# Kernel tuning notes

Hardware: AMD Instinct MI355X
Metric: run time of the kernel (lower is better)

## Reference

```python
import jax, jax.numpy as jnp
import numpy as np

N_NODES = 50000
N_EDGES = 800000
HIDDEN = 128
HEADS = 8
HEAD_DIM = HIDDEN // HEADS
N_LAYERS = 2
BATCH = 64
INPUT = 300


def setup_inputs() -> dict:
    key = jax.random.key(0)
    ks = jax.random.split(key, 10)
    s = 0.05
    word_embed_matrix = jax.random.normal(ks[0], (N_NODES, INPUT), dtype=jnp.float32)
    edge_index = jax.random.randint(ks[1], (2, N_EDGES), 0, N_NODES, dtype=jnp.int32)
    target_idx = jax.random.randint(ks[2], (BATCH,), 0, N_NODES, dtype=jnp.int32)
    # labels: first half positive, second half negative (batch/2 pos as in original loss)
    label_id = jnp.concatenate([jnp.ones(BATCH // 2, jnp.int32), jnp.zeros(BATCH // 2, jnp.int32)])
    lin1_W = jax.random.normal(ks[3], (INPUT, HIDDEN), dtype=jnp.float32) * s
    lin1_b = jnp.zeros((HIDDEN,), jnp.float32)
    gat_W = jax.random.normal(ks[4], (N_LAYERS, HIDDEN, HIDDEN), dtype=jnp.float32) * s
    gat_att_src = jax.random.normal(ks[5], (N_LAYERS, HEADS, HEAD_DIM), dtype=jnp.float32) * s
    gat_att_dst = jax.random.normal(ks[6], (N_LAYERS, HEADS, HEAD_DIM), dtype=jnp.float32) * s
    gat_bias = jnp.zeros((N_LAYERS, HIDDEN), jnp.float32)
    lin3_W = jax.random.normal(ks[7], (HIDDEN, 1), dtype=jnp.float32) * s
    lin3_b = jnp.zeros((1,), jnp.float32)
    return {"word_embed_matrix": word_embed_matrix, "edge_index": edge_index,
            "target_idx": target_idx, "label_id": label_id,
            "lin1_W": lin1_W, "lin1_b": lin1_b, "gat_W": gat_W,
            "gat_att_src": gat_att_src, "gat_att_dst": gat_att_dst,
            "gat_bias": gat_bias, "lin3_W": lin3_W, "lin3_b": lin3_b}


def gat_layer(x, src, dst, W, a_src, a_dst, b):
    # x: [N, HIDDEN]; src/dst: [E'] (self loops included)
    N = x.shape[0]
    h = (x @ W).reshape(N, HEADS, HEAD_DIM)               # [N,H,C]
    alpha_src = jnp.sum(h * a_src, axis=-1)               # [N,H]
    alpha_dst = jnp.sum(h * a_dst, axis=-1)               # [N,H]
    e = jax.nn.leaky_relu(alpha_src[src] + alpha_dst[dst], 0.2)  # [E',H]
    # softmax over incoming edges of each dst node (segment softmax)
    emax = jax.ops.segment_max(e, dst, num_segments=N)    # [N,H]
    ee = jnp.exp(e - emax[dst])
    denom = jax.ops.segment_sum(ee, dst, num_segments=N)  # [N,H]
    alpha = ee / denom[dst]                               # [E',H]
    msg = h[src] * alpha[:, :, None]                      # [E',H,C]
    out = jax.ops.segment_sum(msg, dst, num_segments=N)   # [N,H,C]
    return out.reshape(N, HIDDEN) + b


def reference(word_embed_matrix, edge_index, target_idx, label_id,
              lin1_W, lin1_b, gat_W, gat_att_src, gat_att_dst, gat_bias,
              lin3_W, lin3_b):
    N = word_embed_matrix.shape[0]
    # add self loops (PyG GATConv default)
    loop = jnp.arange(N, dtype=edge_index.dtype)
    src = jnp.concatenate([edge_index[0], loop])
    dst = jnp.concatenate([edge_index[1], loop])
    x = word_embed_matrix @ lin1_W + lin1_b
    for i in range(N_LAYERS):
        x = jax.nn.elu(gat_layer(x, src, dst, gat_W[i], gat_att_src[i], gat_att_dst[i], gat_bias[i]))
    target_embed = x[target_idx]                          # [B, HIDDEN]
    total_score = (target_embed @ lin3_W + lin3_b)[:, 0]  # [B]
    # labels are [1]*B/2 + [0]*B/2 (static layout, matches label_id)
    half = BATCH // 2
    pos_score = total_score[:half]
    neg_score = total_score[half:]
    loss = jnp.mean(jax.nn.relu(1.0 - (pos_score - neg_score)))
    return (total_score, loss)
```

## Files before the change

### kernel.cpp

```cpp
#include <hip/hip_runtime.h>
#include <math.h>

#define N_NODES 50000
#define N_EDGESI 800000
#define E_TOT   850000
#define HIDDEN  128
#define HEADS   8
#define HEAD_DIM 16
#define INPUT   300
#define BATCH   64

#define NR    128
#define RSZ   391
#define CAP   8192
#define CHUNK 2048
#define NSB   ((E_TOT + CHUNK - 1)/CHUNK)
#define FCAP  8192

typedef __bf16 bf16_t;
typedef bf16_t bf16x8 __attribute__((ext_vector_type(8)));
typedef bf16_t bf16x2 __attribute__((ext_vector_type(2)));
typedef float  f32x4  __attribute__((ext_vector_type(4)));
typedef float  f32x2  __attribute__((ext_vector_type(2)));

__global__ void wa_kernel(const float* __restrict__ W, const float* __restrict__ as,
                          const float* __restrict__ ad, float* __restrict__ Wa){
    int k = threadIdx.x;
    #pragma unroll
    for (int j = 0; j < 8; j++){
        float s1 = 0.f, s2 = 0.f;
        #pragma unroll
        for (int d = 0; d < 16; d++){
            float wv = W[k*128 + j*16 + d];
            s1 += wv * as[j*16 + d];
            s2 += wv * ad[j*16 + d];
        }
        Wa[k*16 + j]     = s1;
        Wa[k*16 + 8 + j] = s2;
    }
}

template<int K_REAL, int K_PAD, int NCOL>
__global__ void fused_pack_kernel(const float* __restrict__ W1, const float* __restrict__ Wg,
                                  const float* __restrict__ Wa, const float* __restrict__ b1,
                                  bf16_t* __restrict__ bF, float* __restrict__ bcomb){
    int idx = blockIdx.x*256 + threadIdx.x;
    if (idx < NCOL){
        float s = 0.f;
        for (int d = 0; d < 128; d++)
            s += b1[d] * ((idx < 128) ? Wg[d*128 + idx] : Wa[d*16 + (idx - 128)]);
        bcomb[idx] = s;
    }
    if (idx >= K_PAD*NCOL) return;
    int k = idx / NCOL, col = idx % NCOL;
    float v = 0.f;
    if (k < K_REAL){
        const float* w1r = W1 + k*128;
        if (col < 128){
            for (int m = 0; m < 128; m++) v += w1r[m] * Wg[m*128 + col];
        } else {
            int jj = col - 128;
            for (int m = 0; m < 128; m++) v += w1r[m] * Wa[m*16 + jj];
        }
    }
    int o = ((k >> 3)*NCOL + col)*8 + (k & 7);
    bF[o] = (bf16_t)v;
}

template<int K_REAL, int K_PAD, int NCOL, bool ALPHA>
__global__ void pack_b_kernel(const float* __restrict__ B128, const float* __restrict__ as,
                              const float* __restrict__ ad, bf16_t* __restrict__ bHi){
    int idx = blockIdx.x*256 + threadIdx.x;
    if (idx >= K_PAD*NCOL) return;
    int k = idx / NCOL, col = idx % NCOL;
    float v = 0.f;
    if (k < K_REAL){
        if (!ALPHA || col < 128){
            v = B128[k*128 + col];
        } else {
            int jj = col - 128;
            const float* a = (jj < 8) ? (as + jj*16) : (ad + (jj-8)*16);
            const float* wrow = B128 + k*128 + (jj & 7)*16;
            float s = 0.f;
            #pragma unroll
            for (int d = 0; d < 16; d++) s += wrow[d]*a[d];
            v = s;
        }
    }
    int o = ((k >> 3)*NCOL + col)*8 + (k & 7);
    bHi[o] = (bf16_t)v;
}

template<int K_REAL, int K_PAD, int NT, int GH, int PD, bool A_BF16, bool BIAS_EPI, bool ALPHA, bool OUT8, bool INDIRECT>
__global__ __launch_bounds__(256)
void mfma_gemm6_kernel(const void* __restrict__ A_, const bf16_t* __restrict__ bHi,
                       const float* __restrict__ bias, void* __restrict__ outP,
                       float* __restrict__ asrc_out, float* __restrict__ adst_out, int M,
                       const int* __restrict__ rlist, const int* __restrict__ cnt_ptr)
{
    constexpr int NCOL   = NT * 16;
    constexpr int KSTEPS = K_PAD / 32;
    constexpr int KSPP   = GH / 4;
    constexpr int NPASS  = KSTEPS / KSPP;
    constexpr int PELEM  = GH * NCOL * 8;
    constexpr int SIT    = PELEM / 2048;
    static_assert(KSPP * NPASS == KSTEPS && SIT * 2048 == PELEM, "");
    __shared__ bf16_t blds[PELEM];

    int mEff = M;
    if (INDIRECT) mEff = cnt_ptr[0];
    if ((int)(blockIdx.x*64) >= mEff) return;

    int tid = threadIdx.x, lane = tid & 63, w = tid >> 6;
    int l15 = lane & 15, lg = lane >> 4;
    int m0 = (blockIdx.x*4 + w) * 16;
    int mrow = m0 + l15; if (mrow >= mEff) mrow = mEff - 1;
    int arow_idx = INDIRECT ? rlist[mrow] : mrow;

    const float*  arowF = (const float*) A_ + (size_t)arow_idx*K_REAL;
    const bf16_t* arowB = (const bf16_t*)A_ + (size_t)arow_idx*K_REAL;

    float4 pva[PD], pvb[PD];
    bf16x8 pab[PD];
    #pragma unroll
    for (int i = 0; i < PD; i++){
        int k0 = i*32 + lg*8;
        if (A_BF16){
            pab[i] = *(const bf16x8*)&arowB[k0];
        } else {
            pva[i] = (k0 + 3 < K_REAL) ? *(const float4*)&arowF[k0]     : (float4){0.f,0.f,0.f,0.f};
            pvb[i] = (k0 + 7 < K_REAL) ? *(const float4*)&arowF[k0 + 4] : (float4){0.f,0.f,0.f,0.f};
        }
    }

    f32x4 acc[NT];
    #pragma unroll
    for (int c = 0; c < NT; c++) acc[c] = (f32x4){0.f,0.f,0.f,0.f};

    #pragma unroll
    for (int p = 0; p < NPASS; p++){
        const bf16_t* gB = bHi + (size_t)p*PELEM;
        if (p) __syncthreads();
        #pragma unroll
        for (int it = 0; it < SIT; it++){
            int idx = (tid + it*256)*8;
            *(bf16x8*)&blds[idx] = *(const bf16x8*)&gB[idx];
        }
        __syncthreads();

        #pragma unroll
        for (int i = 0; i < KSPP; i++){
            const int ks = p*KSPP + i;
            const int sl = ks % PD;
            bf16x8 ah;
            if (A_BF16){
                ah = pab[sl];
            } else {
                float4 va = pva[sl], vb = pvb[sl];
                float f[8] = {va.x, va.y, va.z, va.w, vb.x, vb.y, vb.z, vb.w};
                #pragma unroll
                for (int q = 0; q < 8; q++) ah[q] = (bf16_t)f[q];
            }
            if (ks + PD < KSTEPS){
                int k0 = (ks + PD)*32 + lg*8;
                if (A_BF16){
                    pab[sl] = *(const bf16x8*)&arowB[k0];
                } else {
                    pva[sl] = (k0 + 3 < K_REAL) ? *(const float4*)&arowF[k0]     : (float4){0.f,0.f,0.f,0.f};
                    pvb[sl] = (k0 + 7 < K_REAL) ? *(const float4*)&arowF[k0 + 4] : (float4){0.f,0.f,0.f,0.f};
                }
            }
            int gloc = i*4 + lg;
            const bf16_t* b_base = &blds[(gloc*NCOL + l15)*8];
            #pragma unroll
            for (int c = 0; c < NT; c++){
                bf16x8 bh = *(const bf16x8*)&b_base[c*128];
                acc[c] = __builtin_amdgcn_mfma_f32_16x16x32_bf16(ah, bh, acc[c], 0,0,0);
            }
        }
    }

    #pragma unroll
    for (int c = 0; c < 8; c++){
        int col = c*16 + l15;
        float bv = BIAS_EPI ? bias[col] : 0.f;
        #pragma unroll
        for (int r = 0; r < 4; r++){
            int m = m0 + lg*4 + r;
            if (m < mEff){
                int row = INDIRECT ? rlist[m] : m;
                float v = acc[c][r] + bv;
                if (OUT8){
                    int pk = __builtin_amdgcn_cvt_pk_fp8_f32(v, v, 0, false);
                    ((unsigned char*)outP)[(size_t)row*128 + col] = (unsigned char)(pk & 0xff);
                } else {
                    ((bf16_t*)outP)[(size_t)row*128 + col] = (bf16_t)v;
                }
            }
        }
    }
    if (ALPHA){
        float bv8 = BIAS_EPI ? bias[128 + l15] : 0.f;
        #pragma unroll
        for (int r = 0; r < 4; r++){
            int m = m0 + lg*4 + r;
            if (m < mEff){
                int row = INDIRECT ? rlist[m] : m;
                float v = acc[8][r] + bv8;
                if (l15 < 8) asrc_out[row*8 + l15]       = v;
                else         adst_out[row*8 + (l15 - 8)] = v;
            }
        }
    }
}

__global__ void zero_cnt_kernel(int* __restrict__ bucket_cnt){
    bucket_cnt[threadIdx.x] = 0;
}

__global__ __launch_bounds__(256)
void block_sort_kernel(const int* __restrict__ ei, int* __restrict__ bucket_cnt,
                       int2* __restrict__ pairs2){
    __shared__ int2 stageL[CHUNK];
    __shared__ int2 sortedL[CHUNK];
    __shared__ unsigned short binL[CHUNK];
    __shared__ int histL[NR], lstartL[NR], lcurL[NR], gofsL[NR];
    int tid = threadIdx.x, b = blockIdx.x;
    int e0 = b*CHUNK, e1 = e0 + CHUNK; if (e1 > E_TOT) e1 = E_TOT;
    int n = e1 - e0;
    if (tid < NR) histL[tid] = 0;
    __syncthreads();
    for (int i = tid; i < n; i += 256){
        int e = e0 + i;
        int s, d;
        if (e < N_EDGESI){ s = ei[e]; d = ei[N_EDGESI + e]; }
        else { s = e - N_EDGESI; d = s; }
        stageL[i] = make_int2(s, d);
        atomicAdd(&histL[d/RSZ], 1);
    }
    __syncthreads();
    if (tid < NR) lstartL[tid] = histL[tid];
    __syncthreads();
    for (int off = 1; off < NR; off <<= 1){
        int t = 0;
        if (tid < NR && tid >= off) t = lstartL[tid - off];
        __syncthreads();
        if (tid < NR) lstartL[tid] += t;
        __syncthreads();
    }
    if (tid < NR){
        int excl = lstartL[tid] - histL[tid];
        lstartL[tid] = excl;
        lcurL[tid]   = excl;
    }
    __syncthreads();
    for (int i = tid; i < n; i += 256){
        int2 pr = stageL[i];
        int bb = pr.y / RSZ;
        int pos = atomicAdd(&lcurL[bb], 1);
        sortedL[pos] = pr;
        binL[pos] = (unsigned short)bb;
    }
    __syncthreads();
    if (tid < NR) gofsL[tid] = atomicAdd(&bucket_cnt[tid], histL[tid]);
    __syncthreads();
    for (int i = tid; i < n; i += 256){
        int bb = binL[i];
        int dst = bb*CAP + gofsL[bb] + (i - lstartL[bb]);
        pairs2[dst] = sortedL[i];
    }
}

__global__ void rbase_scan_kernel(const int* __restrict__ bucket_cnt, int* __restrict__ rbase){
    __shared__ int s[NR];
    int t = threadIdx.x;
    s[t] = bucket_cnt[t];
    __syncthreads();
    for (int off = 1; off < NR; off <<= 1){
        int u = (t >= off) ? s[t - off] : 0;
        __syncthreads();
        s[t] += u;
        __syncthreads();
    }
    rbase[t + 1] = s[t];
    if (t == 0) rbase[0] = 0;
}

__global__ __launch_bounds__(512)
void csr_finalize_kernel(const int2* __restrict__ pairs2, const int* __restrict__ bucket_cnt,
                         const int* __restrict__ rbase, int* __restrict__ col_src,
                         int* __restrict__ row_ptr){
    __shared__ int2 pairsL[CAP];
    __shared__ int  colL[CAP];
    __shared__ int  degL[512];
    __shared__ int  startL[512];
    __shared__ int  curL[512];
    int tid = threadIdx.x, r = blockIdx.x;
    int cnt = bucket_cnt[r], base = rbase[r];
    degL[tid] = 0;
    __syncthreads();
    for (int i = tid; i < cnt; i += 512){
        int2 pr = pairs2[r*CAP + i];
        pairsL[i] = pr;
        atomicAdd(&degL[pr.y - r*RSZ], 1);
    }
    __syncthreads();
    int v = degL[tid];
    for (int off = 1; off < 512; off <<= 1){
        int u = (tid >= off) ? degL[tid - off] : 0;
        __syncthreads();
        degL[tid] += u;
        __syncthreads();
    }
    int excl = degL[tid] - v;
    startL[tid] = excl;
    curL[tid]   = excl;
    __syncthreads();
    for (int i = tid; i < cnt; i += 512){
        int2 pr = pairsL[i];
        int pos = atomicAdd(&curL[pr.y - r*RSZ], 1);
        colL[pos] = pr.x;
    }
    __syncthreads();
    for (int i = tid; i < cnt; i += 512)
        col_src[base + i] = colL[i];
    if (tid < RSZ){
        int node = r*RSZ + tid;
        if (node < N_NODES) row_ptr[node] = base + startL[tid];
    }
    if (r == NR-1 && tid == 0) row_ptr[N_NODES] = E_TOT;
}

__global__ void build_frontier_kernel(const int* __restrict__ tgt, const int* __restrict__ row_ptr,
                                      const int* __restrict__ col_src, int* __restrict__ list,
                                      int* __restrict__ fcnt){
    __shared__ int st[64], en[64], ofs[65];
    int t = threadIdx.x;
    if (t < 64){ int d = tgt[t]; st[t] = row_ptr[d]; en[t] = row_ptr[d + 1]; }
    __syncthreads();
    if (t == 0){
        int acc = 64;
        for (int i = 0; i < 64; i++){
            ofs[i] = acc;
            int n = en[i] - st[i];
            acc += n;
        }
        if (acc > FCAP) acc = FCAP;
        ofs[64] = acc;
        fcnt[0] = acc;
    }
    __syncthreads();
    if (t < 64) list[t] = tgt[t];
    for (int i = 0; i < 64; i++){
        int n = en[i] - st[i];
        int o = ofs[i];
        for (int j = t; j < n && o + j < FCAP; j += 256)
            list[o + j] = col_src[st[i] + j];
    }
}

__global__ __launch_bounds__(256)
void gat_aggregate_kernel(const int* __restrict__ row_ptr, const int* __restrict__ col_src,
                          const unsigned char* __restrict__ H8, const float* __restrict__ a_s,
                          const float* __restrict__ a_d, const float* __restrict__ bias,
                          bf16_t* __restrict__ xout, const int* __restrict__ nlist, int nn,
                          const int* __restrict__ nn_ptr){
    __shared__ float alds[4][8][65];
    int wave = threadIdx.x >> 6;
    int lane = threadIdx.x & 63;
    if (nn_ptr) nn = nn_ptr[0];
    int gid = blockIdx.x*4 + wave;
    if (gid >= nn) return;
    int d = nlist ? nlist[gid] : gid;
    int start = row_ptr[d], end = row_ptr[d + 1];
    int deg = end - start;
    int hme = lane >> 3, seg = lane & 7;

    float ad_[8];
    {
        float4 t0 = *(const float4*)&a_d[d*8];
        float4 t1 = *(const float4*)&a_d[d*8 + 4];
        ad_[0]=t0.x; ad_[1]=t0.y; ad_[2]=t0.z; ad_[3]=t0.w;
        ad_[4]=t1.x; ad_[5]=t1.y; ad_[6]=t1.z; ad_[7]=t1.w;
    }

    float acc0 = 0.f, acc1 = 0.f, dh;
    unsigned hoff = 2u*lane;

    if (deg <= 64){
        bool act = lane < deg;
        int sreg = 0;
        float e[8];
        #pragma unroll
        for (int h = 0; h < 8; h++) e[h] = 0.f;
        if (act){
            sreg = col_src[start + lane];
            float4 s0 = *(const float4*)&a_s[sreg*8];
            float4 s1 = *(const float4*)&a_s[sreg*8 + 4];
            float as_[8] = {s0.x,s0.y,s0.z,s0.w,s1.x,s1.y,s1.z,s1.w};
            #pragma unroll
            for (int h = 0; h < 8; h++){
                float v = as_[h] + ad_[h];
                v = v > 0.f ? v : 0.2f*v;
                e[h] = __expf(fminf(v, 70.f));
            }
        }
        unsigned rbase = (unsigned)sreg * 128u;
        #pragma unroll
        for (int h = 0; h < 8; h++) alds[wave][h][lane] = e[h];

        const float* row = &alds[wave][hme][0];
        float s = 0.f;
        #pragma unroll
        for (int j = 0; j < 8; j++) s += row[seg*8 + j];
        s += __shfl_xor(s, 1); s += __shfl_xor(s, 2); s += __shfl_xor(s, 4);
        dh = 1.0f / s;

        float acc0b = 0.f, acc1b = 0.f;
        int iters = (deg + 7) >> 3;
        for (int it = 0; it < iters; it++){
            int p = it*8;
            unsigned o0 = __shfl(rbase, p+0) + hoff, o1 = __shfl(rbase, p+1) + hoff;
            unsigned o2 = __shfl(rbase, p+2) + hoff, o3 = __shfl(rbase, p+3) + hoff;
            unsigned o4 = __shfl(rbase, p+4) + hoff, o5 = __shfl(rbase, p+5) + hoff;
            unsigned o6 = __shfl(rbase, p+6) + hoff, o7 = __shfl(rbase, p+7) + hoff;
            unsigned short g0 = *(const unsigned short*)&H8[o0];
            unsigned short g1 = *(const unsigned short*)&H8[o1];
            unsigned short g2 = *(const unsigned short*)&H8[o2];
            unsigned short g3 = *(const unsigned short*)&H8[o3];
            unsigned short g4 = *(const unsigned short*)&H8[o4];
            unsigned short g5 = *(const unsigned short*)&H8[o5];
            unsigned short g6 = *(const unsigned short*)&H8[o6];
            unsigned short g7 = *(const unsigned short*)&H8[o7];
            float a0 = row[p+0], a1 = row[p+1], a2 = row[p+2], a3 = row[p+3];
            float a4 = row[p+4], a5 = row[p+5], a6 = row[p+6], a7 = row[p+7];
            f32x2 f0 = __builtin_amdgcn_cvt_pk_f32_fp8((int)g0, false);
            f32x2 f1 = __builtin_amdgcn_cvt_pk_f32_fp8((int)g1, false);
            f32x2 f2 = __builtin_amdgcn_cvt_pk_f32_fp8((int)g2, false);
            f32x2 f3 = __builtin_amdgcn_cvt_pk_f32_fp8((int)g3, false);
            f32x2 f4 = __builtin_amdgcn_cvt_pk_f32_fp8((int)g4, false);
            f32x2 f5 = __builtin_amdgcn_cvt_pk_f32_fp8((int)g5, false);
            f32x2 f6 = __builtin_amdgcn_cvt_pk_f32_fp8((int)g6, false);
            f32x2 f7 = __builtin_amdgcn_cvt_pk_f32_fp8((int)g7, false);
            acc0  += f0.x*a0 + f2.x*a2;
            acc1  += f0.y*a0 + f2.y*a2;
            acc0b += f1.x*a1 + f3.x*a3;
            acc1b += f1.y*a1 + f3.y*a3;
            acc0  += f4.x*a4 + f6.x*a6;
            acc1  += f4.y*a4 + f6.y*a6;
            acc0b += f5.x*a5 + f7.x*a7;
            acc1b += f5.y*a5 + f7.y*a7;
        }
        acc0 += acc0b;
        acc1 += acc1b;
    } else {
        float adh = ad_[hme];
        float s = 0.f;
        for (int p = start + seg; p < end; p += 8){
            int sn = col_src[p];
            float v = a_s[sn*8 + hme] + adh;
            v = v > 0.f ? v : 0.2f*v;
            s += __expf(fminf(v, 70.f));
        }
        s += __shfl_xor(s, 1); s += __shfl_xor(s, 2); s += __shfl_xor(s, 4);
        dh = 1.0f / s;
        for (int p = start; p < end; p++){
            int sn = col_src[p];
            float v = a_s[sn*8 + hme] + adh;
            v = v > 0.f ? v : 0.2f*v;
            float a = __expf(fminf(v, 70.f));
            unsigned short g = *(const unsigned short*)&H8[(size_t)sn*128 + hoff];
            f32x2 f = __builtin_amdgcn_cvt_pk_f32_fp8((int)g, false);
            acc0 += f.x*a;
            acc1 += f.y*a;
        }
    }

    float o0 = acc0*dh + bias[2*lane];
    float o1 = acc1*dh + bias[2*lane + 1];
    o0 = o0 > 0.f ? o0 : expm1f(o0);
    o1 = o1 > 0.f ? o1 : expm1f(o1);
    bf16x2 o = {(bf16_t)o0, (bf16_t)o1};
    *(bf16x2*)&xout[(size_t)d*HIDDEN + 2*lane] = o;
}

__global__ void head_kernel(const bf16_t* __restrict__ x, const int* __restrict__ tgt,
                            const float* __restrict__ w, const float* __restrict__ b,
                            float* __restrict__ dout){
    int t = threadIdx.x;
    const bf16_t* row = x + (size_t)tgt[t]*HIDDEN;
    float v = 0.f;
    #pragma unroll
    for (int c = 0; c < HIDDEN; c += 8){
        bf16x8 xv = *(const bf16x8*)&row[c];
        #pragma unroll
        for (int j = 0; j < 8; j++) v += (float)xv[j] * w[c + j];
    }
    float sc = v + b[0];
    dout[t] = sc;
    float neg = __shfl(sc, t + 32);
    float dlt = 1.0f - (sc - neg);
    float term = (t < 32) ? (dlt > 0.f ? dlt : 0.f) : 0.f;
    #pragma unroll
    for (int m = 32; m >= 1; m >>= 1) term += __shfl_xor(term, m);
    if (t == 0) dout[BATCH] = term * (1.0f/32.0f);
}

extern "C" void kernel_launch(void* const* d_in, const int* in_sizes, int n_in,
                              void* d_out, int out_size, void* d_ws, size_t ws_size,
                              hipStream_t stream) {
    const float* word   = (const float*)d_in[0];
    const int*   ei     = (const int*)  d_in[1];
    const int*   tgt    = (const int*)  d_in[2];
    const float* lin1W  = (const float*)d_in[4];
    const float* lin1b  = (const float*)d_in[5];
    const float* gatW   = (const float*)d_in[6];
    const float* attS   = (const float*)d_in[7];
    const float* attD   = (const float*)d_in[8];
    const float* gatB   = (const float*)d_in[9];
    const float* lin3W  = (const float*)d_in[10];
    const float* lin3b  = (const float*)d_in[11];

    char* ws = (char*)d_ws;
    size_t off = 0;
    bf16_t*        Xb       = (bf16_t*)(ws + off);        off += (size_t)N_NODES*HIDDEN*2;
    unsigned char* H8       = (unsigned char*)(ws + off); off += (size_t)N_NODES*HIDDEN;
    off = (off + 15) & ~(size_t)15;
    float*   a_s       = (float*)(ws + off);   off += (size_t)N_NODES*HEADS*4;
    float*   a_d       = (float*)(ws + off);   off += (size_t)N_NODES*HEADS*4;
    int*     row_ptr   = (int*)(ws + off);     off += (size_t)(N_NODES + 16)*4;
    int*     col_src   = (int*)(ws + off);     off += (size_t)E_TOT*4;
    int*     bucket_cnt= (int*)(ws + off);     off += 512;
    int*     rbase     = (int*)(ws + off);     off += 1024;
    int*     frontier  = (int*)(ws + off);     off += (size_t)FCAP*4;
    int*     fcnt      = (int*)(ws + off);     off += 64;
    int2*    pairs2    = (int2*)(ws + off);    off += (size_t)NR*CAP*8;
    bf16_t*  bF        = (bf16_t*)(ws + off);  off += (size_t)384*144*2;
    float*   Wa0       = (float*)(ws + off);   off += 128*16*4;
    float*   bcomb     = (float*)(ws + off);   off += 256;
    bf16_t*  b2        = (bf16_t*)(ws + off);  off += (size_t)128*144*2;

    const int GB = ((N_NODES + 15)/16 + 3)/4;
    const int FB = FCAP/64;

    zero_cnt_kernel    <<<1, NR, 0, stream>>>(bucket_cnt);
    block_sort_kernel  <<<NSB, 256, 0, stream>>>(ei, bucket_cnt, pairs2);
    rbase_scan_kernel  <<<1, NR, 0, stream>>>(bucket_cnt, rbase);
    csr_finalize_kernel<<<NR, 512, 0, stream>>>(pairs2, bucket_cnt, rbase, col_src, row_ptr);
    build_frontier_kernel<<<1, 256, 0, stream>>>(tgt, row_ptr, col_src, frontier, fcnt);

    const float* Wg0 = gatW;
    wa_kernel<<<1, 128, 0, stream>>>(Wg0, attS, attD, Wa0);
    fused_pack_kernel<INPUT, 384, 144><<<(384*144 + 255)/256, 256, 0, stream>>>(
        lin1W, Wg0, Wa0, lin1b, bF, bcomb);
    mfma_gemm6_kernel<INPUT, 384, 9, 16, 5, false, true, true, true, false><<<GB, 256, 0, stream>>>(
        word, bF, bcomb, H8, a_s, a_d, N_NODES, nullptr, nullptr);
    gat_aggregate_kernel<<<FCAP/4, 256, 0, stream>>>(
        row_ptr, col_src, H8, a_s, a_d, gatB, Xb, frontier, 0, fcnt);

    {
        const float* W = gatW + (size_t)HIDDEN*HIDDEN;
        pack_b_kernel<HIDDEN, 128, 144, true><<<(128*144 + 255)/256, 256, 0, stream>>>(
            W, attS + HEADS*HEAD_DIM, attD + HEADS*HEAD_DIM, b2);
        mfma_gemm6_kernel<HIDDEN, 128, 9, 16, 4, true, false, true, true, true><<<FB, 256, 0, stream>>>(
            Xb, b2, nullptr, H8, a_s, a_d, N_NODES, frontier, fcnt);
        gat_aggregate_kernel<<<(BATCH + 3)/4, 256, 0, stream>>>(
            row_ptr, col_src, H8, a_s, a_d, gatB + HIDDEN, Xb, tgt, BATCH, nullptr);
    }

    head_kernel<<<1, 64, 0, stream>>>(Xb, tgt, lin3W, lin3b, (float*)d_out);
}
```

Before: 123.4 us.

## Restrict first-layer projection GEMM to the two-hop neighborhood of targets

Adds a second frontier-building kernel that expands the one-hop frontier into its in-neighbors (two-hop receptive field) using an atomic counter. The first fused lin1+GAT projection GEMM then runs only over that list instead of all 50k nodes, since only those rows feed the layer-1 aggregation for frontier nodes. This trades a full GEMM over all nodes for an extra small kernel plus gathered rows. If the two-hop set overflows its 32768-entry cap, edges are silently dropped, and rows may be computed redundantly because the list is not deduplicated.

```diff
diff --git a/kernel.cpp b/kernel.cpp
--- a/kernel.cpp
+++ b/kernel.cpp
@@ -16,6 +16,7 @@
 #define CHUNK 2048
 #define NSB   ((E_TOT + CHUNK - 1)/CHUNK)
 #define FCAP  8192
+#define FCAP2 32768
 
 typedef __bf16 bf16_t;
 typedef bf16_t bf16x8 __attribute__((ext_vector_type(8)));
@@ -342,12 +343,12 @@
         int acc = 64;
         for (int i = 0; i < 64; i++){
             ofs[i] = acc;
-            int n = en[i] - st[i];
-            acc += n;
+            acc += en[i] - st[i];
         }
         if (acc > FCAP) acc = FCAP;
         ofs[64] = acc;
         fcnt[0] = acc;
+        fcnt[1] = acc;
     }
     __syncthreads();
     if (t < 64) list[t] = tgt[t];
@@ -357,6 +358,25 @@
         for (int j = t; j < n && o + j < FCAP; j += 256)
             list[o + j] = col_src[st[i] + j];
     }
+}
+
+__global__ __launch_bounds__(256)
+void build_frontier2_kernel(const int* __restrict__ frontier, int* __restrict__ fcnt,
+                            const int* __restrict__ row_ptr, const int* __restrict__ col_src,
+                            int* __restrict__ list2){
+    int nf = fcnt[0];
+    int wave = blockIdx.x*4 + (threadIdx.x >> 6);
+    int lane = threadIdx.x & 63;
+    if (wave >= nf) return;
+    int d = frontier[wave];
+    list2[wave] = d;
+    int st = row_ptr[d], en = row_ptr[d + 1], n = en - st;
+    int pos = 0;
+    if (lane == 0) pos = atomicAdd(&fcnt[1], n);
+    pos = __shfl(pos, 0);
+    if (pos + n > FCAP2) return;
+    for (int j = lane; j < n; j += 64)
+        list2[pos + j] = col_src[st + j];
 }
 
 __global__ __launch_bounds__(256)
@@ -533,6 +553,7 @@
     int*     bucket_cnt= (int*)(ws + off);     off += 512;
     int*     rbase     = (int*)(ws + off);     off += 1024;
     int*     frontier  = (int*)(ws + off);     off += (size_t)FCAP*4;
+    int*     list2     = (int*)(ws + off);     off += (size_t)FCAP2*4;
     int*     fcnt      = (int*)(ws + off);     off += 64;
     int2*    pairs2    = (int2*)(ws + off);    off += (size_t)NR*CAP*8;
     bf16_t*  bF        = (bf16_t*)(ws + off);  off += (size_t)384*144*2;
@@ -540,21 +561,22 @@
     float*   bcomb     = (float*)(ws + off);   off += 256;
     bf16_t*  b2        = (bf16_t*)(ws + off);  off += (size_t)128*144*2;
 
-    const int GB = ((N_NODES + 15)/16 + 3)/4;
-    const int FB = FCAP/64;
+    const int FB  = FCAP/64;
+    const int F2B = FCAP2/64;
 
     zero_cnt_kernel    <<<1, NR, 0, stream>>>(bucket_cnt);
     block_sort_kernel  <<<NSB, 256, 0, stream>>>(ei, bucket_cnt, pairs2);
     rbase_scan_kernel  <<<1, NR, 0, stream>>>(bucket_cnt, rbase);
     csr_finalize_kernel<<<NR, 512, 0, stream>>>(pairs2, bucket_cnt, rbase, col_src, row_ptr);
     build_frontier_kernel<<<1, 256, 0, stream>>>(tgt, row_ptr, col_src, frontier, fcnt);
+    build_frontier2_kernel<<<FCAP/4, 256, 0, stream>>>(frontier, fcnt, row_ptr, col_src, list2);
 
     const float* Wg0 = gatW;
     wa_kernel<<<1, 128, 0, stream>>>(Wg0, attS, attD, Wa0);
     fused_pack_kernel<INPUT, 384, 144><<<(384*144 + 255)/256, 256, 0, stream>>>(
         lin1W, Wg0, Wa0, lin1b, bF, bcomb);
-    mfma_gemm6_kernel<INPUT, 384, 9, 16, 5, false, true, true, true, false><<<GB, 256, 0, stream>>>(
-        word, bF, bcomb, H8, a_s, a_d, N_NODES, nullptr, nullptr);
+    mfma_gemm6_kernel<INPUT, 384, 9, 16, 5, false, true, true, true, true><<<F2B, 256, 0, stream>>>(
+        word, bF, bcomb, H8, a_s, a_d, N_NODES, list2, fcnt + 1);
     gat_aggregate_kernel<<<FCAP/4, 256, 0, stream>>>(
         row_ptr, col_src, H8, a_s, a_d, gatB, Xb, frontier, 0, fcnt);
 
```

Measured after the change: 135.2 us. 9.5% more time.
